# Performance work log

Hardware: AMD Instinct MI355X
Metric: run time of the kernel (lower is better)

The kernel has to match this reference:

```python
import jax, jax.numpy as jnp
import numpy as np

B, DIM, H, W = 16, 256, 64, 64
HEADS, DHEAD, MEM = 4, 32, 4
HIDDEN = HEADS * DHEAD


def setup_inputs() -> dict:
    key = jax.random.key(0)
    ks = jax.random.split(key, 4)
    return {
        "x": jax.random.normal(ks[0], (B, DIM, H, W), dtype=jnp.float32),
        "g1": jnp.ones((DIM,), dtype=jnp.float32),
        "w_qkv": jax.random.normal(ks[1], (3 * HIDDEN, DIM), dtype=jnp.float32) * 0.02,
        "mem_kv": jax.random.normal(ks[2], (2, HEADS, DHEAD, MEM), dtype=jnp.float32),
        "w_out": jax.random.normal(ks[3], (DIM, HIDDEN), dtype=jnp.float32) * 0.02,
        "b_out": jnp.zeros((DIM,), dtype=jnp.float32),
        "g2": jnp.ones((DIM,), dtype=jnp.float32),
    }


def _rmsnorm(x, g):
    # F.normalize(x, dim=1) * g * sqrt(dim); g broadcast over (1, dim, 1, 1)
    n = jnp.sqrt(jnp.sum(x * x, axis=1, keepdims=True))
    scale = jnp.asarray(x.shape[1], x.dtype) ** 0.5
    return x / jnp.maximum(n, 1e-12) * g[None, :, None, None] * scale


def reference(x, g1, w_qkv, mem_kv, w_out, b_out, g2):
    b, c, h, w = x.shape
    attn_scale = DHEAD ** -0.5
    xn = _rmsnorm(x, g1)
    # 1x1 conv == channel matmul; chunk(3, dim=1) -> leading axis 3 after reshape
    qkv = jnp.einsum('oc,bchw->bohw', w_qkv, xn)
    qkv = qkv.reshape(b, 3, HEADS, DHEAD, h * w)  # b 3 h d n
    q, k, v = qkv[:, 0], qkv[:, 1], qkv[:, 2]
    mk = jnp.broadcast_to(mem_kv[0][None], (b, HEADS, DHEAD, MEM))
    mv = jnp.broadcast_to(mem_kv[1][None], (b, HEADS, DHEAD, MEM))
    k = jnp.concatenate([mk, k], axis=-1)  # b h d (m+n)
    v = jnp.concatenate([mv, v], axis=-1)
    q = jax.nn.softmax(q, axis=-2) * attn_scale  # softmax over feature dim d
    k = jax.nn.softmax(k, axis=-1)               # softmax over token dim n
    context = jnp.einsum('bhdn,bhen->bhde', k, v)  # d x e per head
    out = jnp.einsum('bhde,bhdn->bhen', context, q)
    out = out.reshape(b, HIDDEN, h, w)
    out = jnp.einsum('oc,bchw->bohw', w_out, out) + b_out[None, :, None, None]
    return _rmsnorm(out, g2)
```

## Files before the change

### kernel.cpp

```cpp
#include <hip/hip_runtime.h>
#include <hip/hip_bf16.h>

#define NB 16
#define DIM 256
#define HW 4096
#define HEADS 4
#define DHEAD 32
#define MEM 4
#define HIDDEN 128

typedef __hip_bfloat16 bf16;
typedef __attribute__((ext_vector_type(8))) short bf16x8;
typedef __attribute__((ext_vector_type(4))) float f32x4;
typedef __attribute__((ext_vector_type(4))) unsigned short us4;

#define AS1 __attribute__((address_space(1)))
#define AS3 __attribute__((address_space(3)))

__device__ __forceinline__ void gld_lds16(const void* g, void* l) {
    __builtin_amdgcn_global_load_lds((const AS1 void*)g, (AS3 void*)l, 16, 0, 0);
}
__device__ __forceinline__ float b2f(short s) {
    union { unsigned int u; float f; } x; x.u = ((unsigned int)(unsigned short)s) << 16; return x.f;
}
__device__ __forceinline__ short f2bs(float f) {
    bf16 h = __float2bfloat16(f);
    return *reinterpret_cast<short*>(&h);
}

constexpr size_t OFF_W1B  = 0;
constexpr size_t OFF_PCTX = OFF_W1B + 98304*2;
constexpr size_t OFF_CTXN = OFF_PCTX + (size_t)64*64*1056*4;
constexpr size_t OFF_M    = OFF_CTXN + (size_t)64*1024*4;
constexpr size_t OFF_QT   = OFF_M + (size_t)NB*DIM*HIDDEN*2;

__global__ void k_prep(const float* __restrict__ wqkv, const float* __restrict__ g1,
                       short* __restrict__ w1b) {
    int i = blockIdx.x * 256 + threadIdx.x;
    w1b[i] = f2bs(wqkv[i] * g1[i & (DIM - 1)]);
}

__global__ __launch_bounds__(384) void k_fused(const short* __restrict__ w1b,
                                               const float* __restrict__ x,
                                               short* __restrict__ qT,
                                               float* __restrict__ pctx) {
    int nt = blockIdx.x, b = blockIdx.y;
    int n0 = nt * 64;
    __shared__ char smem[65536];
    short* As = (short*)smem;
    short* Bs = (short*)(smem + 49152);
    short* xs = (short*)(smem + 57344);
    int t = threadIdx.x;
    int w = t >> 6, lane = t & 63;
    int lr = lane & 15, lg = lane >> 4;
    const f32x4 fz = {0.f, 0.f, 0.f, 0.f};
    f32x4 acc[4][4];
#pragma unroll
    for (int m = 0; m < 4; ++m)
#pragma unroll
        for (int n = 0; n < 4; ++n) acc[m][n] = fz;
    f32x4 ssv = fz;
    const float* xb = x + (size_t)b * DIM * HW + n0;

    for (int kk = 0; kk < 256; kk += 64) {
        __syncthreads();
#pragma unroll
        for (int is = 0; is < 8; ++is) {
            int o = is * 6144 + t * 16;
            int row = o >> 7;
            int js = ((o >> 4) & 7) ^ (row & 7);
            gld_lds16(w1b + (size_t)row * 256 + kk + js * 8, smem + o);
        }
        if (t < 256) {
            int rr = t >> 4, cc = (t & 15) * 4;
#pragma unroll
            for (int p = 0; p < 4; ++p) {
                int c = rr + p * 16;
                f32x4 v4 = *(const f32x4*)(xb + (size_t)(kk + c) * HW + cc);
                us4 h4;
#pragma unroll
                for (int j = 0; j < 4; ++j) { ssv[j] += v4[j] * v4[j]; h4[j] = (unsigned short)f2bs(v4[j]); }
                *(us4*)(xs + c * 64 + cc) = h4;
            }
        }
        __syncthreads();
        if (t < 256) {
            int n = t & 63, cq = t >> 6;
            alignas(16) short tmp[16];
#pragma unroll
            for (int i = 0; i < 16; ++i) tmp[i] = xs[(cq * 16 + i) * 64 + n];
            *(bf16x8*)(Bs + n * 64 + (((cq * 2)     ^ (n & 7)) << 3)) = *(bf16x8*)tmp;
            *(bf16x8*)(Bs + n * 64 + (((cq * 2 + 1) ^ (n & 7)) << 3)) = *(bf16x8*)(tmp + 8);
        }
        __syncthreads();
#pragma unroll
        for (int ks = 0; ks < 2; ++ks) {
            bf16x8 av[4], bv[4];
            int j = lg + 4 * ks;
#pragma unroll
            for (int m = 0; m < 4; ++m) {
                int row = w * 64 + m * 16 + lr;
                av[m] = *(const bf16x8*)(As + row * 64 + ((j ^ (row & 7)) << 3));
            }
#pragma unroll
            for (int n = 0; n < 4; ++n) {
                int row = n * 16 + lr;
                bv[n] = *(const bf16x8*)(Bs + row * 64 + ((j ^ (row & 7)) << 3));
            }
#pragma unroll
            for (int m = 0; m < 4; ++m)
#pragma unroll
                for (int n = 0; n < 4; ++n)
                    acc[m][n] = __builtin_amdgcn_mfma_f32_16x16x32_bf16(av[m], bv[n], acc[m][n], 0, 0, 0);
        }
    }
    __syncthreads();
    float* ssp = (float*)(smem + 32768);
    float* r2s = (float*)(smem + 36864);
    short* ekb = (short*)smem;
    short* vb  = (short*)(smem + 16384);
    if (t < 256) *(f32x4*)(ssp + (t >> 4) * 64 + (t & 15) * 4) = ssv;
    __syncthreads();
    if (t < 64) {
        float s = 0.f;
#pragma unroll
        for (int g = 0; g < 16; ++g) s += ssp[g * 64 + t];
        r2s[t] = 16.0f / fmaxf(sqrtf(s), 1e-12f);
    }
    __syncthreads();
    float rv[4];
#pragma unroll
    for (int nf = 0; nf < 4; ++nf) rv[nf] = r2s[nf * 16 + lr];

    if (w < 2) {
#pragma unroll
        for (int nf = 0; nf < 4; ++nf) {
            int gcol = n0 + nf * 16 + lr;
#pragma unroll
            for (int a = 0; a < 2; ++a) {
                float v[8];
#pragma unroll
                for (int mm = 0; mm < 2; ++mm)
#pragma unroll
                    for (int q = 0; q < 4; ++q)
                        v[mm * 4 + q] = acc[2 * a + mm][nf][q] * rv[nf];
                float mx = v[0];
#pragma unroll
                for (int i = 1; i < 8; ++i) mx = fmaxf(mx, v[i]);
                mx = fmaxf(mx, __shfl_xor(mx, 16));
                mx = fmaxf(mx, __shfl_xor(mx, 32));
                float sum = 0.f;
#pragma unroll
                for (int i = 0; i < 8; ++i) { v[i] = __expf(v[i] - mx); sum += v[i]; }
                sum += __shfl_xor(sum, 16);
                sum += __shfl_xor(sum, 32);
                float inv = 0.17677669529663689f / sum;
                size_t base = ((size_t)b * HW + gcol) * 128 + (w * 2 + a) * 32 + lg * 4;
#pragma unroll
                for (int mm = 0; mm < 2; ++mm) {
                    us4 pk;
#pragma unroll
                    for (int q = 0; q < 4; ++q)
                        pk[q] = (unsigned short)f2bs(v[mm * 4 + q] * inv);
                    *(us4*)(qT + base + mm * 16) = pk;
                }
            }
        }
    } else if (w < 4) {
#pragma unroll
        for (int m = 0; m < 4; ++m)
#pragma unroll
            for (int nf = 0; nf < 4; ++nf)
#pragma unroll
                for (int q = 0; q < 4; ++q) {
                    int rloc = (w - 2) * 64 + m * 16 + lg * 4 + q;
                    ekb[rloc * 64 + nf * 16 + lr] = f2bs(__expf(acc[m][nf][q] * rv[nf]));
                }
    } else {
#pragma unroll
        for (int m = 0; m < 4; ++m)
#pragma unroll
            for (int nf = 0; nf < 4; ++nf)
#pragma unroll
                for (int q = 0; q < 4; ++q) {
                    int rloc = (w - 4) * 64 + m * 16 + lg * 4 + q;
                    vb[rloc * 64 + nf * 16 + lr] = f2bs(acc[m][nf][q] * rv[nf]);
                }
    }
    __syncthreads();
    if (w < 4) {
        int h = w;
        f32x4 c2[2][2];
        c2[0][0] = fz; c2[0][1] = fz; c2[1][0] = fz; c2[1][1] = fz;
#pragma unroll
        for (int ks = 0; ks < 2; ++ks) {
            int j = lg + 4 * ks;
            bf16x8 a2[2], b2[2];
#pragma unroll
            for (int mm = 0; mm < 2; ++mm)
                a2[mm] = *(const bf16x8*)(ekb + (h * 32 + mm * 16 + lr) * 64 + j * 8);
#pragma unroll
            for (int nn = 0; nn < 2; ++nn)
                b2[nn] = *(const bf16x8*)(vb + (h * 32 + nn * 16 + lr) * 64 + j * 8);
#pragma unroll
            for (int mm = 0; mm < 2; ++mm)
#pragma unroll
                for (int nn = 0; nn < 2; ++nn)
                    c2[mm][nn] = __builtin_amdgcn_mfma_f32_16x16x32_bf16(a2[mm], b2[nn], c2[mm][nn], 0, 0, 0);
        }
        float* o = pctx + ((size_t)nt * 64 + b * 4 + h) * 1056;
#pragma unroll
        for (int mm = 0; mm < 2; ++mm)
#pragma unroll
            for (int nn = 0; nn < 2; ++nn)
#pragma unroll
                for (int qq = 0; qq < 4; ++qq) {
                    int d = mm * 16 + lg * 4 + qq;
                    int e = nn * 16 + lr;
                    o[d * 32 + e] = c2[mm][nn][qq];
                }
    } else {
        int hd = (w - 4) * 64 + lane;
        float rs = 0.f;
#pragma unroll
        for (int blk = 0; blk < 8; ++blk) {
            bf16x8 e8 = *(const bf16x8*)(ekb + hd * 64 + blk * 8);
#pragma unroll
            for (int j = 0; j < 8; ++j) rs += b2f(e8[j]);
        }
        pctx[((size_t)nt * 64 + b * 4 + (hd >> 5)) * 1056 + 1024 + (hd & 31)] = rs;
    }
}

__global__ __launch_bounds__(256) void k_red(const float* __restrict__ pctx,
                                             const float* __restrict__ memkv,
                                             float* __restrict__ ctxn) {
    int ds = blockIdx.x, bh = blockIdx.y;
    int t = threadIdx.x;
    int dd = t >> 5, ee = t & 31;
    int d = ds * 8 + dd;
    int h = bh & 3;
    __shared__ float rss[8];
    float s = 0.f;
#pragma unroll 8
    for (int c = 0; c < 64; ++c)
        s += pctx[((size_t)c * 64 + bh) * 1056 + d * 32 + ee];
    if (t < 8) {
        int d2 = ds * 8 + t;
        float rs = 0.f;
#pragma unroll 8
        for (int c = 0; c < 64; ++c)
            rs += pctx[((size_t)c * 64 + bh) * 1056 + 1024 + d2];
#pragma unroll
        for (int m2 = 0; m2 < MEM; ++m2) rs += __expf(memkv[(h * 32 + d2) * MEM + m2]);
        rss[t] = rs;
    }
    float mem = 0.f;
#pragma unroll
    for (int m2 = 0; m2 < MEM; ++m2)
        mem += __expf(memkv[(h * 32 + d) * MEM + m2]) * memkv[512 + (h * 32 + ee) * MEM + m2];
    __syncthreads();
    ctxn[(size_t)bh * 1024 + d * 32 + ee] = (s + mem) / rss[dd];
}

__global__ __launch_bounds__(256) void k_M2(const float* __restrict__ ctxn,
                                            const float* __restrict__ wout,
                                            short* __restrict__ Mmat) {
    int og = blockIdx.x, b = blockIdx.y;
    __shared__ float ctx[4 * 33 * 33];
    __shared__ float wsw[32 * 136];
    int t = threadIdx.x;
#pragma unroll
    for (int j = 0; j < 16; ++j) {
        int e = t + j * 256;
        int h = e >> 10, dd = (e >> 5) & 31, ee = e & 31;
        ctx[h * 1089 + dd * 33 + ee] = ctxn[(size_t)(b * 4 + h) * 1024 + (e & 1023)];
    }
#pragma unroll
    for (int j = 0; j < 4; ++j) {
        int e4 = t + j * 256;
        int row = e4 >> 5, c = (e4 & 31) * 4;
        f32x4 w4 = *(const f32x4*)(wout + (size_t)(og * 32 + row) * HIDDEN + c);
        *(f32x4*)(wsw + row * 136 + (c >> 5) * 34 + (c & 31)) = w4;
    }
    __syncthreads();
    int ol = t >> 3, hg = t & 7;
    alignas(16) short out16[16];
#pragma unroll
    for (int ii = 0; ii < 16; ++ii) {
        int hd = hg * 16 + ii;
        int h = hd >> 5, dd = hd & 31;
        float s = 0.f;
#pragma unroll
        for (int e = 0; e < 32; ++e)
            s += wsw[ol * 136 + h * 34 + e] * ctx[h * 1089 + dd * 33 + e];
        out16[ii] = f2bs(s);
    }
    short* op = Mmat + ((size_t)(b * 256 + og * 32 + ol)) * 128 + hg * 16;
    *(bf16x8*)(op)     = *(bf16x8*)(out16);
    *(bf16x8*)(op + 8) = *(bf16x8*)(out16 + 8);
}

__global__ __launch_bounds__(256) void k_out2(const short* __restrict__ Mmat,
                                              const short* __restrict__ qT,
                                              const float* __restrict__ bout,
                                              const float* __restrict__ g2,
                                              float* __restrict__ out) {
    int nt = blockIdx.x, b = blockIdx.y;
    __shared__ short As[256 * 64];
    __shared__ short Bs[64 * 64];
    __shared__ float sw[4][80];
    __shared__ float r2s[64];
    int t = threadIdx.x;
    int wave = t >> 6, lane = t & 63;
    int lr = lane & 15, lg = lane >> 4;
    const short* Ag = Mmat + (size_t)b * 256 * 128;
    const short* Bg = qT + ((size_t)b * HW + nt * 64) * 128;
    const f32x4 fz = {0.f, 0.f, 0.f, 0.f};
    f32x4 acc[4][4];
#pragma unroll
    for (int m = 0; m < 4; ++m)
#pragma unroll
        for (int n = 0; n < 4; ++n) acc[m][n] = fz;

    for (int kk = 0; kk < 128; kk += 64) {
        if (kk) __syncthreads();
#pragma unroll
        for (int is = 0; is < 8; ++is) {
            int o = is * 4096 + t * 16;
            int rr2 = o >> 7;
            int js = ((o >> 4) & 7) ^ (rr2 & 7);
            gld_lds16(Ag + (size_t)rr2 * 128 + kk + js * 8, (char*)As + o);
        }
#pragma unroll
        for (int is = 0; is < 2; ++is) {
            int o = is * 4096 + t * 16;
            int rr2 = o >> 7;
            int js = ((o >> 4) & 7) ^ (rr2 & 7);
            gld_lds16(Bg + (size_t)rr2 * 128 + kk + js * 8, (char*)Bs + o);
        }
        __syncthreads();
#pragma unroll
        for (int ks = 0; ks < 2; ++ks) {
            bf16x8 av[4], bv[4];
            int j = lg + 4 * ks;
#pragma unroll
            for (int m = 0; m < 4; ++m) {
                int row = wave * 64 + m * 16 + lr;
                av[m] = *(const bf16x8*)((const char*)As + row * 128 + ((j ^ (row & 7)) << 4));
            }
#pragma unroll
            for (int n = 0; n < 4; ++n) {
                int row = n * 16 + lr;
                bv[n] = *(const bf16x8*)((const char*)Bs + row * 128 + ((j ^ (row & 7)) << 4));
            }
#pragma unroll
            for (int m = 0; m < 4; ++m)
#pragma unroll
                for (int n = 0; n < 4; ++n)
                    acc[m][n] = __builtin_amdgcn_mfma_f32_16x16x32_bf16(av[m], bv[n], acc[m][n], 0, 0, 0);
        }
    }
    float bb[4][4], gg[4][4];
#pragma unroll
    for (int m = 0; m < 4; ++m)
#pragma unroll
        for (int q = 0; q < 4; ++q) {
            int row = wave * 64 + m * 16 + lg * 4 + q;
            bb[m][q] = bout[row];
            gg[m][q] = g2[row];
        }
    float ssn[4] = {0.f, 0.f, 0.f, 0.f};
#pragma unroll
    for (int n = 0; n < 4; ++n)
#pragma unroll
        for (int m = 0; m < 4; ++m)
#pragma unroll
            for (int q = 0; q < 4; ++q) {
                float val = acc[m][n][q] + bb[m][q];
                acc[m][n][q] = val;
                ssn[n] += val * val;
            }
#pragma unroll
    for (int n = 0; n < 4; ++n) {
        ssn[n] += __shfl_xor(ssn[n], 16);
        ssn[n] += __shfl_xor(ssn[n], 32);
    }
    if (lg == 0) {
#pragma unroll
        for (int n = 0; n < 4; ++n) sw[wave][n * 16 + lr] = ssn[n];
    }
    __syncthreads();
    if (t < 64) {
        float s = sw[0][t] + sw[1][t] + sw[2][t] + sw[3][t];
        r2s[t] = 16.0f / fmaxf(sqrtf(s), 1e-12f);
    }
    __syncthreads();
    float* op = out + (size_t)b * DIM * HW + nt * 64;
#pragma unroll
    for (int n = 0; n < 4; ++n) {
        float rc = r2s[n * 16 + lr];
#pragma unroll
        for (int m = 0; m < 4; ++m)
#pragma unroll
            for (int q = 0; q < 4; ++q) {
                int row = wave * 64 + m * 16 + lg * 4 + q;
                op[(size_t)row * HW + n * 16 + lr] = acc[m][n][q] * rc * gg[m][q];
            }
    }
}

extern "C" void kernel_launch(void* const* d_in, const int* in_sizes, int n_in,
                              void* d_out, int out_size, void* d_ws, size_t ws_size,
                              hipStream_t stream) {
    const float* x     = (const float*)d_in[0];
    const float* g1    = (const float*)d_in[1];
    const float* wqkv  = (const float*)d_in[2];
    const float* memkv = (const float*)d_in[3];
    const float* wout  = (const float*)d_in[4];
    const float* bout  = (const float*)d_in[5];
    const float* g2    = (const float*)d_in[6];
    float* out = (float*)d_out;
    char* ws = (char*)d_ws;

    short* w1b  = (short*)(ws + OFF_W1B);
    float* pctx = (float*)(ws + OFF_PCTX);
    float* ctxn = (float*)(ws + OFF_CTXN);
    short* Mmat = (short*)(ws + OFF_M);
    short* qT   = (short*)(ws + OFF_QT);

    k_prep<<<384, 256, 0, stream>>>(wqkv, g1, w1b);
    k_fused<<<dim3(64, NB), 384, 0, stream>>>(w1b, x, qT, pctx);
    k_red<<<dim3(4, 64), 256, 0, stream>>>(pctx, memkv, ctxn);
    k_M2<<<dim3(8, NB), 256, 0, stream>>>(ctxn, wout, Mmat);
    k_out2<<<dim3(64, NB), 256, 0, stream>>>(Mmat, qT, bout, g2, out);
}
```

Before: 81.20 us.

## Double-buffer QKV projection K-loop with register-staged x transpose

Restructures the fused QKV GEMM main loop from 64-wide K tiles with three barriers per step into 32-wide K tiles that are double-buffered in LDS, with one barrier per step. The x tile is loaded into registers ahead of time and written straight into the transposed B layout, which drops the intermediate xs staging buffer and the separate transpose pass. Shared memory shrinks to 56KB and launch bounds now request 4 blocks. The goal is to overlap global loads with MFMA work and cut barrier overhead. The cost is more loop iterations and extra register pressure from the prefetched values.

```diff
diff --git a/kernel.cpp b/kernel.cpp
--- a/kernel.cpp
+++ b/kernel.cpp
@@ -40,16 +40,16 @@
     w1b[i] = f2bs(wqkv[i] * g1[i & (DIM - 1)]);
 }
 
-__global__ __launch_bounds__(384) void k_fused(const short* __restrict__ w1b,
-                                               const float* __restrict__ x,
-                                               short* __restrict__ qT,
-                                               float* __restrict__ pctx) {
+__global__ __launch_bounds__(384, 4) void k_fused(const short* __restrict__ w1b,
+                                                  const float* __restrict__ x,
+                                                  short* __restrict__ qT,
+                                                  float* __restrict__ pctx) {
+    constexpr int AS_SZ  = 24576;
+    constexpr int BS_OFF = 49152;
+    constexpr int BS_SZ  = 4096;
+    __shared__ char smem[57344];
     int nt = blockIdx.x, b = blockIdx.y;
-    int n0 = nt * 64;
-    __shared__ char smem[65536];
-    short* As = (short*)smem;
-    short* Bs = (short*)(smem + 49152);
-    short* xs = (short*)(smem + 57344);
+    int n0g = nt * 64;
     int t = threadIdx.x;
     int w = t >> 6, lane = t & 63;
     int lr = lane & 15, lg = lane >> 4;
@@ -60,82 +60,102 @@
 #pragma unroll
         for (int n = 0; n < 4; ++n) acc[m][n] = fz;
     f32x4 ssv = fz;
-    const float* xb = x + (size_t)b * DIM * HW + n0;
-
-    for (int kk = 0; kk < 256; kk += 64) {
+
+    int n0 = 4 * (t & 15);
+    int c0 = 2 * (t >> 4);
+    const float* xb = x + (size_t)b * DIM * HW + n0g + n0;
+    float xv[2][4];
+
+    auto STAGE_LOAD = [&](int kt, int buf) {
+        int kk = kt * 32;
+#pragma unroll
+        for (int is = 0; is < 4; ++is) {
+            int o = is * 6144 + t * 16;
+            int row = o >> 6;
+            int js = ((o >> 4) & 3) ^ (row & 3);
+            gld_lds16(w1b + (size_t)row * 256 + kk + js * 8, smem + buf * AS_SZ + o);
+        }
+        if (t < 256) {
+#pragma unroll
+            for (int i = 0; i < 2; ++i) {
+                f32x4 v4 = *(const f32x4*)(xb + (size_t)(kk + c0 + i) * HW);
+#pragma unroll
+                for (int j = 0; j < 4; ++j) xv[i][j] = v4[j];
+            }
+        }
+    };
+    auto STAGE_WRITE = [&](int buf) {
+        if (t < 256) {
+            char* bsb = smem + BS_OFF + buf * BS_SZ;
+#pragma unroll
+            for (int j = 0; j < 4; ++j) {
+                float a = xv[0][j], c = xv[1][j];
+                ssv[j] += a * a + c * c;
+                int row = n0 + j;
+                int rot = ((row >> 2) ^ (row >> 4)) & 3;
+                int phys = ((c0 >> 3) + rot) & 3;
+                unsigned int pk = ((unsigned int)(unsigned short)f2bs(c) << 16)
+                                  | (unsigned short)f2bs(a);
+                *(unsigned int*)(bsb + row * 64 + phys * 16 + ((c0 * 2) & 15)) = pk;
+            }
+        }
+    };
+    auto MFMA_STEP = [&](int buf) {
+        bf16x8 av[4], bv[4];
+        const char* ab = smem + buf * AS_SZ;
+        const char* bb = smem + BS_OFF + buf * BS_SZ;
+#pragma unroll
+        for (int m = 0; m < 4; ++m) {
+            int row = w * 64 + m * 16 + lr;
+            av[m] = *(const bf16x8*)(ab + row * 64 + ((lg ^ (row & 3)) << 4));
+        }
+#pragma unroll
+        for (int nf = 0; nf < 4; ++nf) {
+            int row = nf * 16 + lr;
+            int rot = ((row >> 2) ^ (row >> 4)) & 3;
+            bv[nf] = *(const bf16x8*)(bb + row * 64 + (((lg + rot) & 3) << 4));
+        }
+#pragma unroll
+        for (int m = 0; m < 4; ++m)
+#pragma unroll
+            for (int nf = 0; nf < 4; ++nf)
+                acc[m][nf] = __builtin_amdgcn_mfma_f32_16x16x32_bf16(av[m], bv[nf], acc[m][nf], 0, 0, 0);
+    };
+
+    STAGE_LOAD(0, 0);
+    STAGE_WRITE(0);
+    __syncthreads();
+#pragma unroll
+    for (int kt = 0; kt < 8; ++kt) {
+        int buf = kt & 1;
+        if (kt < 7) STAGE_LOAD(kt + 1, buf ^ 1);
+        MFMA_STEP(buf);
+        if (kt < 7) STAGE_WRITE(buf ^ 1);
         __syncthreads();
-#pragma unroll
-        for (int is = 0; is < 8; ++is) {
-            int o = is * 6144 + t * 16;
-            int row = o >> 7;
-            int js = ((o >> 4) & 7) ^ (row & 7);
-            gld_lds16(w1b + (size_t)row * 256 + kk + js * 8, smem + o);
-        }
-        if (t < 256) {
-            int rr = t >> 4, cc = (t & 15) * 4;
-#pragma unroll
-            for (int p = 0; p < 4; ++p) {
-                int c = rr + p * 16;
-                f32x4 v4 = *(const f32x4*)(xb + (size_t)(kk + c) * HW + cc);
-                us4 h4;
-#pragma unroll
-                for (int j = 0; j < 4; ++j) { ssv[j] += v4[j] * v4[j]; h4[j] = (unsigned short)f2bs(v4[j]); }
-                *(us4*)(xs + c * 64 + cc) = h4;
-            }
-        }
-        __syncthreads();
-        if (t < 256) {
-            int n = t & 63, cq = t >> 6;
-            alignas(16) short tmp[16];
-#pragma unroll
-            for (int i = 0; i < 16; ++i) tmp[i] = xs[(cq * 16 + i) * 64 + n];
-            *(bf16x8*)(Bs + n * 64 + (((cq * 2)     ^ (n & 7)) << 3)) = *(bf16x8*)tmp;
-            *(bf16x8*)(Bs + n * 64 + (((cq * 2 + 1) ^ (n & 7)) << 3)) = *(bf16x8*)(tmp + 8);
-        }
-        __syncthreads();
-#pragma unroll
-        for (int ks = 0; ks < 2; ++ks) {
-            bf16x8 av[4], bv[4];
-            int j = lg + 4 * ks;
-#pragma unroll
-            for (int m = 0; m < 4; ++m) {
-                int row = w * 64 + m * 16 + lr;
-                av[m] = *(const bf16x8*)(As + row * 64 + ((j ^ (row & 7)) << 3));
-            }
-#pragma unroll
-            for (int n = 0; n < 4; ++n) {
-                int row = n * 16 + lr;
-                bv[n] = *(const bf16x8*)(Bs + row * 64 + ((j ^ (row & 7)) << 3));
-            }
-#pragma unroll
-            for (int m = 0; m < 4; ++m)
-#pragma unroll
-                for (int n = 0; n < 4; ++n)
-                    acc[m][n] = __builtin_amdgcn_mfma_f32_16x16x32_bf16(av[m], bv[n], acc[m][n], 0, 0, 0);
-        }
-    }
-    __syncthreads();
-    float* ssp = (float*)(smem + 32768);
-    float* r2s = (float*)(smem + 36864);
+    }
+
+    float* ssp = (float*)(smem + 49152);
+    float* r2s = (float*)(smem + 53248);
+    if (t < 256) *(f32x4*)(ssp + (t >> 4) * 64 + (t & 15) * 4) = ssv;
+    __syncthreads();
+    if (t < 64) {
+        float s = 0.f;
+#pragma unroll
+        for (int g = 0; g < 16; ++g) s += ssp[g * 64 + t];
+        r2s[t] = 16.0f / fmaxf(sqrtf(s), 1e-12f);
+    }
+    __syncthreads();
+    float rv[4];
+#pragma unroll
+    for (int nf = 0; nf < 4; ++nf) rv[nf] = r2s[nf * 16 + lr];
+
     short* ekb = (short*)smem;
     short* vb  = (short*)(smem + 16384);
-    if (t < 256) *(f32x4*)(ssp + (t >> 4) * 64 + (t & 15) * 4) = ssv;
-    __syncthreads();
-    if (t < 64) {
-        float s = 0.f;
-#pragma unroll
-        for (int g = 0; g < 16; ++g) s += ssp[g * 64 + t];
-        r2s[t] = 16.0f / fmaxf(sqrtf(s), 1e-12f);
-    }
-    __syncthreads();
-    float rv[4];
-#pragma unroll
-    for (int nf = 0; nf < 4; ++nf) rv[nf] = r2s[nf * 16 + lr];
 
     if (w < 2) {
 #pragma unroll
         for (int nf = 0; nf < 4; ++nf) {
-            int gcol = n0 + nf * 16 + lr;
+            int gcol = n0g + nf * 16 + lr;
 #pragma unroll
             for (int a = 0; a < 2; ++a) {
                 float v[8];
```

New measurement: 85.41 us. 1.05x slower.

## Double-buffer x tile in LDS, read weights directly from global, drop transpose pass

Applied to the files above, without the earlier changes.

Restructures the QKV GEMM main loop. The x tile is prefetched into registers and written transposed straight into a double-buffered LDS B tile, which removes the separate transpose staging pass and two of the three barriers per k-step. The weight A operand is now read directly from global memory (L2-resident) instead of being staged into LDS, which shrinks shared memory from 64KB to about 37KB for better occupancy. The cost is that global-latency A loads now sit on the MFMA critical path.

```diff
diff --git a/kernel.cpp b/kernel.cpp
--- a/kernel.cpp
+++ b/kernel.cpp
@@ -13,6 +13,7 @@
 typedef __attribute__((ext_vector_type(8))) short bf16x8;
 typedef __attribute__((ext_vector_type(4))) float f32x4;
 typedef __attribute__((ext_vector_type(4))) unsigned short us4;
+typedef __attribute__((ext_vector_type(2))) unsigned int u32x2;
 
 #define AS1 __attribute__((address_space(1)))
 #define AS3 __attribute__((address_space(3)))
@@ -44,12 +45,9 @@
                                                const float* __restrict__ x,
                                                short* __restrict__ qT,
                                                float* __restrict__ pctx) {
+    __shared__ __align__(16) char smem[37120];
     int nt = blockIdx.x, b = blockIdx.y;
-    int n0 = nt * 64;
-    __shared__ char smem[65536];
-    short* As = (short*)smem;
-    short* Bs = (short*)(smem + 49152);
-    short* xs = (short*)(smem + 57344);
+    int n0g = nt * 64;
     int t = threadIdx.x;
     int w = t >> 6, lane = t & 63;
     int lr = lane & 15, lg = lane >> 4;
@@ -60,82 +58,90 @@
 #pragma unroll
         for (int n = 0; n < 4; ++n) acc[m][n] = fz;
     f32x4 ssv = fz;
-    const float* xb = x + (size_t)b * DIM * HW + n0;
-
-    for (int kk = 0; kk < 256; kk += 64) {
+
+    int c0 = 4 * (t & 15);
+    int n0 = 4 * ((t >> 4) & 15);
+    const float* xb = x + (size_t)b * DIM * HW + n0g + n0;
+    f32x4 xv[4];
+
+    auto XLOAD = [&](int kt) {
+        if (t < 256) {
+#pragma unroll
+            for (int i = 0; i < 4; ++i)
+                xv[i] = *(const f32x4*)(xb + (size_t)(kt * 64 + c0 + i) * HW);
+        }
+    };
+    auto BWRITE = [&](int buf) {
+        if (t < 256) {
+            char* bsb = smem + buf * 8192;
+#pragma unroll
+            for (int j = 0; j < 4; ++j) {
+                int n = n0 + j;
+                float v0 = xv[0][j], v1 = xv[1][j], v2 = xv[2][j], v3 = xv[3][j];
+                ssv[j] += v0 * v0 + v1 * v1 + v2 * v2 + v3 * v3;
+                u32x2 pk;
+                pk[0] = ((unsigned int)(unsigned short)f2bs(v1) << 16) | (unsigned short)f2bs(v0);
+                pk[1] = ((unsigned int)(unsigned short)f2bs(v3) << 16) | (unsigned short)f2bs(v2);
+                int off = n * 128 + (((c0 >> 3) ^ (n & 7)) << 4) + ((c0 >> 2) & 1) * 8;
+                *(u32x2*)(bsb + off) = pk;
+            }
+        }
+    };
+    auto MFMA_STEP = [&](int kt, int buf) {
+        const char* bb = smem + buf * 8192;
+#pragma unroll
+        for (int ks = 0; ks < 2; ++ks) {
+            int j = lg + 4 * ks;
+            bf16x8 av[4], bv[4];
+#pragma unroll
+            for (int m = 0; m < 4; ++m)
+                av[m] = *(const bf16x8*)(w1b + (size_t)(w * 64 + m * 16 + lr) * 256 + kt * 64 + j * 8);
+#pragma unroll
+            for (int nf = 0; nf < 4; ++nf) {
+                int row = nf * 16 + lr;
+                bv[nf] = *(const bf16x8*)(bb + row * 128 + ((j ^ (row & 7)) << 4));
+            }
+#pragma unroll
+            for (int m = 0; m < 4; ++m)
+#pragma unroll
+                for (int nf = 0; nf < 4; ++nf)
+                    acc[m][nf] = __builtin_amdgcn_mfma_f32_16x16x32_bf16(av[m], bv[nf], acc[m][nf], 0, 0, 0);
+        }
+    };
+
+    XLOAD(0);
+    BWRITE(0);
+    __syncthreads();
+#pragma unroll
+    for (int kt = 0; kt < 4; ++kt) {
+        if (kt < 3) XLOAD(kt + 1);
+        MFMA_STEP(kt, kt & 1);
+        if (kt < 3) BWRITE((kt + 1) & 1);
         __syncthreads();
-#pragma unroll
-        for (int is = 0; is < 8; ++is) {
-            int o = is * 6144 + t * 16;
-            int row = o >> 7;
-            int js = ((o >> 4) & 7) ^ (row & 7);
-            gld_lds16(w1b + (size_t)row * 256 + kk + js * 8, smem + o);
-        }
-        if (t < 256) {
-            int rr = t >> 4, cc = (t & 15) * 4;
-#pragma unroll
-            for (int p = 0; p < 4; ++p) {
-                int c = rr + p * 16;
-                f32x4 v4 = *(const f32x4*)(xb + (size_t)(kk + c) * HW + cc);
-                us4 h4;
-#pragma unroll
-                for (int j = 0; j < 4; ++j) { ssv[j] += v4[j] * v4[j]; h4[j] = (unsigned short)f2bs(v4[j]); }
-                *(us4*)(xs + c * 64 + cc) = h4;
-            }
-        }
-        __syncthreads();
-        if (t < 256) {
-            int n = t & 63, cq = t >> 6;
-            alignas(16) short tmp[16];
-#pragma unroll
-            for (int i = 0; i < 16; ++i) tmp[i] = xs[(cq * 16 + i) * 64 + n];
-            *(bf16x8*)(Bs + n * 64 + (((cq * 2)     ^ (n & 7)) << 3)) = *(bf16x8*)tmp;
-            *(bf16x8*)(Bs + n * 64 + (((cq * 2 + 1) ^ (n & 7)) << 3)) = *(bf16x8*)(tmp + 8);
-        }
-        __syncthreads();
-#pragma unroll
-        for (int ks = 0; ks < 2; ++ks) {
-            bf16x8 av[4], bv[4];
-            int j = lg + 4 * ks;
-#pragma unroll
-            for (int m = 0; m < 4; ++m) {
-                int row = w * 64 + m * 16 + lr;
-                av[m] = *(const bf16x8*)(As + row * 64 + ((j ^ (row & 7)) << 3));
-            }
-#pragma unroll
-            for (int n = 0; n < 4; ++n) {
-                int row = n * 16 + lr;
-                bv[n] = *(const bf16x8*)(Bs + row * 64 + ((j ^ (row & 7)) << 3));
-            }
-#pragma unroll
-            for (int m = 0; m < 4; ++m)
-#pragma unroll
-                for (int n = 0; n < 4; ++n)
-                    acc[m][n] = __builtin_amdgcn_mfma_f32_16x16x32_bf16(av[m], bv[n], acc[m][n], 0, 0, 0);
-        }
-    }
-    __syncthreads();
+    }
+
     float* ssp = (float*)(smem + 32768);
     float* r2s = (float*)(smem + 36864);
+    if (t < 256) *(f32x4*)(ssp + (t & 15) * 64 + n0) = ssv;
+    __syncthreads();
+    if (t < 64) {
+        float s = 0.f;
+#pragma unroll
+        for (int g = 0; g < 16; ++g) s += ssp[g * 64 + t];
+        r2s[t] = 16.0f / fmaxf(sqrtf(s), 1e-12f);
+    }
+    __syncthreads();
+    float rv[4];
+#pragma unroll
+    for (int nf = 0; nf < 4; ++nf) rv[nf] = r2s[nf * 16 + lr];
+
     short* ekb = (short*)smem;
     short* vb  = (short*)(smem + 16384);
-    if (t < 256) *(f32x4*)(ssp + (t >> 4) * 64 + (t & 15) * 4) = ssv;
-    __syncthreads();
-    if (t < 64) {
-        float s = 0.f;
-#pragma unroll
-        for (int g = 0; g < 16; ++g) s += ssp[g * 64 + t];
-        r2s[t] = 16.0f / fmaxf(sqrtf(s), 1e-12f);
-    }
-    __syncthreads();
-    float rv[4];
-#pragma unroll
-    for (int nf = 0; nf < 4; ++nf) rv[nf] = r2s[nf * 16 + lr];
 
     if (w < 2) {
 #pragma unroll
         for (int nf = 0; nf < 4; ++nf) {
-            int gcol = n0 + nf * 16 + lr;
+            int gcol = n0g + nf * 16 + lr;
 #pragma unroll
             for (int a = 0; a < 2; ++a) {
                 float v[8];
```

Result: slower. 93.56 us (+15.2%).

## Split x transpose and norm into separate kernels; widen QKV GEMM tile to 128 tokens

Applied to the files above, without the earlier changes.

Adds a pre-pass kernel that converts x to bf16 in token-major layout and computes partial sums of squares, plus a small kernel that turns those sums into per-token RMS scales. The main QKV GEMM then loads both operands straight into LDS with global_load_lds and uses 768 threads over 128-token tiles. This halves the number of partial contexts that k_red has to reduce. It removes the in-kernel transpose and the extra syncs, but adds two launches and a bf16 round trip of x through global memory.

```diff
diff --git a/kernel.cpp b/kernel.cpp
--- a/kernel.cpp
+++ b/kernel.cpp
@@ -29,10 +29,13 @@
 }
 
 constexpr size_t OFF_W1B  = 0;
-constexpr size_t OFF_PCTX = OFF_W1B + 98304*2;
-constexpr size_t OFF_CTXN = OFF_PCTX + (size_t)64*64*1056*4;
+constexpr size_t OFF_R    = OFF_W1B + 98304*2;
+constexpr size_t OFF_RP   = OFF_R + 65536*4;
+constexpr size_t OFF_PCTX = OFF_RP + 4*65536*4;
+constexpr size_t OFF_CTXN = OFF_PCTX + (size_t)32*64*1056*4;
 constexpr size_t OFF_M    = OFF_CTXN + (size_t)64*1024*4;
 constexpr size_t OFF_QT   = OFF_M + (size_t)NB*DIM*HIDDEN*2;
+constexpr size_t OFF_XT   = OFF_QT + (size_t)NB*HW*HIDDEN*2;
 
 __global__ void k_prep(const float* __restrict__ wqkv, const float* __restrict__ g1,
                        short* __restrict__ w1b) {
@@ -40,18 +43,53 @@
     w1b[i] = f2bs(wqkv[i] * g1[i & (DIM - 1)]);
 }
 
-__global__ __launch_bounds__(384) void k_fused(const short* __restrict__ w1b,
-                                               const float* __restrict__ x,
-                                               short* __restrict__ qT,
-                                               float* __restrict__ pctx) {
+__global__ __launch_bounds__(256) void k_tr(const float* __restrict__ x,
+                                            short* __restrict__ xT,
+                                            float* __restrict__ rpart) {
+    int n0 = blockIdx.x * 64, cy = blockIdx.y, b = blockIdx.z;
+    int c0 = cy * 64;
+    __shared__ short xs[64 * 65];
+    __shared__ float ps[4][64];
+    int t = threadIdx.x;
+    int ln = t & 63, cb = t >> 6;
+    const float* xp = x + ((size_t)b * DIM + c0) * HW + n0;
+    float ss = 0.f;
+#pragma unroll
+    for (int j = 0; j < 16; ++j) {
+        int c = cb * 16 + j;
+        float v = xp[(size_t)c * HW + ln];
+        ss += v * v;
+        xs[c * 65 + ln] = f2bs(v);
+    }
+    ps[cb][ln] = ss;
+    __syncthreads();
+    if (t < 64)
+        rpart[((size_t)cy * NB + b) * HW + n0 + t] = ps[0][t] + ps[1][t] + ps[2][t] + ps[3][t];
+    int n = t >> 2, ch = t & 3;
+    alignas(16) short tmp[16];
+#pragma unroll
+    for (int i = 0; i < 16; ++i) tmp[i] = xs[(ch * 16 + i) * 65 + n];
+    short* o = xT + ((size_t)b * HW + n0 + n) * DIM + c0 + ch * 16;
+    *(bf16x8*)(o)     = *(bf16x8*)(tmp);
+    *(bf16x8*)(o + 8) = *(bf16x8*)(tmp + 8);
+}
+
+__global__ void k_rfin(const float* __restrict__ rpart, float* __restrict__ r) {
+    int i = blockIdx.x * 256 + threadIdx.x;
+    float s = rpart[i] + rpart[65536 + i] + rpart[131072 + i] + rpart[196608 + i];
+    r[i] = 16.0f / fmaxf(sqrtf(s), 1e-12f);
+}
+
+__global__ __launch_bounds__(768) void k_gemm(const short* __restrict__ w1b,
+                                              const short* __restrict__ xT,
+                                              const float* __restrict__ r,
+                                              short* __restrict__ qT,
+                                              float* __restrict__ pctx) {
+    __shared__ __align__(16) char smem[65536];
     int nt = blockIdx.x, b = blockIdx.y;
-    int n0 = nt * 64;
-    __shared__ char smem[65536];
-    short* As = (short*)smem;
-    short* Bs = (short*)(smem + 49152);
-    short* xs = (short*)(smem + 57344);
     int t = threadIdx.x;
     int w = t >> 6, lane = t & 63;
+    int wr = w >> 1, wc = w & 1;
     int lr = lane & 15, lg = lane >> 4;
     const f32x4 fz = {0.f, 0.f, 0.f, 0.f};
     f32x4 acc[4][4];
@@ -59,83 +97,67 @@
     for (int m = 0; m < 4; ++m)
 #pragma unroll
         for (int n = 0; n < 4; ++n) acc[m][n] = fz;
-    f32x4 ssv = fz;
-    const float* xb = x + (size_t)b * DIM * HW + n0;
-
-    for (int kk = 0; kk < 256; kk += 64) {
-        __syncthreads();
-#pragma unroll
-        for (int is = 0; is < 8; ++is) {
-            int o = is * 6144 + t * 16;
+
+    const short* Bg = xT + ((size_t)b * HW + nt * 128) * 256;
+
+    for (int kt = 0; kt < 4; ++kt) {
+        int kk = kt * 64;
+        if (kt) __syncthreads();
+#pragma unroll
+        for (int is = 0; is < 4; ++is) {
+            int o = is * 12288 + t * 16;
             int row = o >> 7;
             int js = ((o >> 4) & 7) ^ (row & 7);
             gld_lds16(w1b + (size_t)row * 256 + kk + js * 8, smem + o);
         }
+        {
+            int o = t * 16;
+            int row = o >> 7;
+            int js = ((o >> 4) & 7) ^ (row & 7);
+            gld_lds16(Bg + (size_t)row * 256 + kk + js * 8, smem + 49152 + o);
+        }
         if (t < 256) {
-            int rr = t >> 4, cc = (t & 15) * 4;
-#pragma unroll
-            for (int p = 0; p < 4; ++p) {
-                int c = rr + p * 16;
-                f32x4 v4 = *(const f32x4*)(xb + (size_t)(kk + c) * HW + cc);
-                us4 h4;
-#pragma unroll
-                for (int j = 0; j < 4; ++j) { ssv[j] += v4[j] * v4[j]; h4[j] = (unsigned short)f2bs(v4[j]); }
-                *(us4*)(xs + c * 64 + cc) = h4;
-            }
+            int o = 12288 + t * 16;
+            int row = o >> 7;
+            int js = ((o >> 4) & 7) ^ (row & 7);
+            gld_lds16(Bg + (size_t)row * 256 + kk + js * 8, smem + 49152 + o);
         }
         __syncthreads();
-        if (t < 256) {
-            int n = t & 63, cq = t >> 6;
-            alignas(16) short tmp[16];
-#pragma unroll
-            for (int i = 0; i < 16; ++i) tmp[i] = xs[(cq * 16 + i) * 64 + n];
-            *(bf16x8*)(Bs + n * 64 + (((cq * 2)     ^ (n & 7)) << 3)) = *(bf16x8*)tmp;
-            *(bf16x8*)(Bs + n * 64 + (((cq * 2 + 1) ^ (n & 7)) << 3)) = *(bf16x8*)(tmp + 8);
-        }
-        __syncthreads();
 #pragma unroll
         for (int ks = 0; ks < 2; ++ks) {
+            int j = lg + 4 * ks;
             bf16x8 av[4], bv[4];
-            int j = lg + 4 * ks;
 #pragma unroll
             for (int m = 0; m < 4; ++m) {
-                int row = w * 64 + m * 16 + lr;
-                av[m] = *(const bf16x8*)(As + row * 64 + ((j ^ (row & 7)) << 3));
-            }
-#pragma unroll
-            for (int n = 0; n < 4; ++n) {
-                int row = n * 16 + lr;
-                bv[n] = *(const bf16x8*)(Bs + row * 64 + ((j ^ (row & 7)) << 3));
+                int row = wr * 64 + m * 16 + lr;
+                av[m] = *(const bf16x8*)(smem + row * 128 + ((j ^ (row & 7)) << 4));
+            }
+#pragma unroll
+            for (int nf = 0; nf < 4; ++nf) {
+                int row = wc * 64 + nf * 16 + lr;
+                bv[nf] = *(const bf16x8*)(smem + 49152 + row * 128 + ((j ^ (row & 7)) << 4));
             }
 #pragma unroll
             for (int m = 0; m < 4; ++m)
 #pragma unroll
-                for (int n = 0; n < 4; ++n)
-                    acc[m][n] = __builtin_amdgcn_mfma_f32_16x16x32_bf16(av[m], bv[n], acc[m][n], 0, 0, 0);
-        }
-    }
-    __syncthreads();
-    float* ssp = (float*)(smem + 32768);
-    float* r2s = (float*)(smem + 36864);
+                for (int nf = 0; nf < 4; ++nf)
+                    acc[m][nf] = __builtin_amdgcn_mfma_f32_16x16x32_bf16(av[m], bv[nf], acc[m][nf], 0, 0, 0);
+        }
+    }
+
+    int gcol0 = nt * 128 + wc * 64 + lr;
+    float rv[4];
+#pragma unroll
+    for (int nf = 0; nf < 4; ++nf) rv[nf] = r[(size_t)b * HW + gcol0 + nf * 16];
+
+    __syncthreads();
     short* ekb = (short*)smem;
-    short* vb  = (short*)(smem + 16384);
-    if (t < 256) *(f32x4*)(ssp + (t >> 4) * 64 + (t & 15) * 4) = ssv;
-    __syncthreads();
-    if (t < 64) {
-        float s = 0.f;
-#pragma unroll
-        for (int g = 0; g < 16; ++g) s += ssp[g * 64 + t];
-        r2s[t] = 16.0f / fmaxf(sqrtf(s), 1e-12f);
-    }
-    __syncthreads();
-    float rv[4];
-#pragma unroll
-    for (int nf = 0; nf < 4; ++nf) rv[nf] = r2s[nf * 16 + lr];
-
-    if (w < 2) {
+    short* vb  = (short*)(smem + 32768);
+
+    if (wr < 2) {
 #pragma unroll
         for (int nf = 0; nf < 4; ++nf) {
-            int gcol = n0 + nf * 16 + lr;
+            int gcol = gcol0 + nf * 16;
 #pragma unroll
             for (int a = 0; a < 2; ++a) {
                 float v[8];
@@ -155,7 +177,7 @@
                 sum += __shfl_xor(sum, 16);
                 sum += __shfl_xor(sum, 32);
                 float inv = 0.17677669529663689f / sum;
-                size_t base = ((size_t)b * HW + gcol) * 128 + (w * 2 + a) * 32 + lg * 4;
+                size_t base = ((size_t)b * HW + gcol) * 128 + (wr * 2 + a) * 32 + lg * 4;
 #pragma unroll
                 for (int mm = 0; mm < 2; ++mm) {
                     us4 pk;
@@ -166,15 +188,17 @@
                 }
             }
         }
-    } else if (w < 4) {
+    } else if (wr < 4) {
 #pragma unroll
         for (int m = 0; m < 4; ++m)
 #pragma unroll
             for (int nf = 0; nf < 4; ++nf)
 #pragma unroll
                 for (int q = 0; q < 4; ++q) {
-                    int rloc = (w - 2) * 64 + m * 16 + lg * 4 + q;
-                    ekb[rloc * 64 + nf * 16 + lr] = f2bs(__expf(acc[m][nf][q] * rv[nf]));
+                    int rloc = (wr - 2) * 64 + m * 16 + lg * 4 + q;
+                    int col = wc * 64 + nf * 16 + lr;
+                    int cs = ((((col >> 3) ^ (rloc & 15)) << 3) | (col & 7));
+                    ekb[rloc * 128 + cs] = f2bs(__expf(acc[m][nf][q] * rv[nf]));
                 }
     } else {
 #pragma unroll
@@ -183,8 +207,10 @@
             for (int nf = 0; nf < 4; ++nf)
 #pragma unroll
                 for (int q = 0; q < 4; ++q) {
-                    int rloc = (w - 4) * 64 + m * 16 + lg * 4 + q;
-                    vb[rloc * 64 + nf * 16 + lr] = f2bs(acc[m][nf][q] * rv[nf]);
+                    int rloc = (wr - 4) * 64 + m * 16 + lg * 4 + q;
+                    int col = wc * 64 + nf * 16 + lr;
+                    int cs = ((((col >> 3) ^ (rloc & 15)) << 3) | (col & 7));
+                    vb[rloc * 128 + cs] = f2bs(acc[m][nf][q] * rv[nf]);
                 }
     }
     __syncthreads();
@@ -193,15 +219,19 @@
         f32x4 c2[2][2];
         c2[0][0] = fz; c2[0][1] = fz; c2[1][0] = fz; c2[1][1] = fz;
 #pragma unroll
-        for (int ks = 0; ks < 2; ++ks) {
-            int j = lg + 4 * ks;
+        for (int ks = 0; ks < 4; ++ks) {
+            int j = ks * 4 + lg;
             bf16x8 a2[2], b2[2];
 #pragma unroll
-            for (int mm = 0; mm < 2; ++mm)
-                a2[mm] = *(const bf16x8*)(ekb + (h * 32 + mm * 16 + lr) * 64 + j * 8);
-#pragma unroll
-            for (int nn = 0; nn < 2; ++nn)
-                b2[nn] = *(const bf16x8*)(vb + (h * 32 + nn * 16 + lr) * 64 + j * 8);
+            for (int mm = 0; mm < 2; ++mm) {
+                int row = h * 32 + mm * 16 + lr;
+                a2[mm] = *(const bf16x8*)(ekb + row * 128 + ((j ^ (row & 15)) << 3));
+            }
+#pragma unroll
+            for (int nn = 0; nn < 2; ++nn) {
+                int row = h * 32 + nn * 16 + lr;
+                b2[nn] = *(const bf16x8*)(vb + row * 128 + ((j ^ (row & 15)) << 3));
+            }
 #pragma unroll
             for (int mm = 0; mm < 2; ++mm)
 #pragma unroll
@@ -219,16 +249,20 @@
                     int e = nn * 16 + lr;
                     o[d * 32 + e] = c2[mm][nn][qq];
                 }
-    } else {
-        int hd = (w - 4) * 64 + lane;
+    } else if (w >= 8) {
+        int hd = (w - 8) * 32 + (lane & 31);
+        int half = lane >> 5;
         float rs = 0.f;
 #pragma unroll
         for (int blk = 0; blk < 8; ++blk) {
-            bf16x8 e8 = *(const bf16x8*)(ekb + hd * 64 + blk * 8);
-#pragma unroll
-            for (int j = 0; j < 8; ++j) rs += b2f(e8[j]);
-        }
-        pctx[((size_t)nt * 64 + b * 4 + (hd >> 5)) * 1056 + 1024 + (hd & 31)] = rs;
+            int chunk = half * 8 + blk;
+            bf16x8 e8 = *(const bf16x8*)(ekb + hd * 128 + ((chunk ^ (hd & 15)) << 3));
+#pragma unroll
+            for (int jj = 0; jj < 8; ++jj) rs += b2f(e8[jj]);
+        }
+        rs += __shfl_xor(rs, 32);
+        if (lane < 32)
+            pctx[((size_t)nt * 64 + b * 4 + (w - 8)) * 1056 + 1024 + (lane & 31)] = rs;
     }
 }
 
@@ -243,13 +277,13 @@
     __shared__ float rss[8];
     float s = 0.f;
 #pragma unroll 8
-    for (int c = 0; c < 64; ++c)
+    for (int c = 0; c < 32; ++c)
         s += pctx[((size_t)c * 64 + bh) * 1056 + d * 32 + ee];
     if (t < 8) {
         int d2 = ds * 8 + t;
         float rs = 0.f;
 #pragma unroll 8
-        for (int c = 0; c < 64; ++c)
+        for (int c = 0; c < 32; ++c)
             rs += pctx[((size_t)c * 64 + bh) * 1056 + 1024 + d2];
 #pragma unroll
         for (int m2 = 0; m2 < MEM; ++m2) rs += __expf(memkv[(h * 32 + d2) * MEM + m2]);
@@ -424,13 +458,18 @@
     char* ws = (char*)d_ws;
 
     short* w1b  = (short*)(ws + OFF_W1B);
+    float* r    = (float*)(ws + OFF_R);
+    float* rpart= (float*)(ws + OFF_RP);
     float* pctx = (float*)(ws + OFF_PCTX);
     float* ctxn = (float*)(ws + OFF_CTXN);
     short* Mmat = (short*)(ws + OFF_M);
     short* qT   = (short*)(ws + OFF_QT);
+    short* xT   = (short*)(ws + OFF_XT);
 
     k_prep<<<384, 256, 0, stream>>>(wqkv, g1, w1b);
-    k_fused<<<dim3(64, NB), 384, 0, stream>>>(w1b, x, qT, pctx);
+    k_tr<<<dim3(64, 4, NB), 256, 0, stream>>>(x, xT, rpart);
+    k_rfin<<<256, 256, 0, stream>>>(rpart, r);
+    k_gemm<<<dim3(32, NB), 768, 0, stream>>>(w1b, xT, r, qT, pctx);
     k_red<<<dim3(4, 64), 256, 0, stream>>>(pctx, memkv, ctxn);
     k_M2<<<dim3(8, NB), 256, 0, stream>>>(ctxn, wout, Mmat);
     k_out2<<<dim3(64, NB), 256, 0, stream>>>(Mmat, qT, bout, g2, out);
```

After: 80.18 us. About the same (-1.3%).
